# Performance work log

Hardware: AMD Instinct MI355X
Metric: run time of the kernel (lower is better)

The kernel has to match this reference:

```python
import jax, jax.numpy as jnp
import numpy as np

# Geometry constants fixed by the source's index arithmetic
GRID_P, GRID_Q, NUM_ANCH = 60, 40, 9   # p = (i//9)%60, q = i//(60*9), sr = i%9
N = GRID_P * GRID_Q * NUM_ANCH          # 21600 anchors per image
K = 1000                                # top-K candidates kept before NMS
MAX_BOXES = 18                          # fixed output boxes per image
THRESH = 0.5                            # NMS overlap threshold
BATCH = 64


def setup_inputs() -> dict:
    key = jax.random.key(0)
    k1, k2 = jax.random.split(key)
    x = jax.random.normal(k1, (BATCH, N, 6), dtype=jnp.float32)
    # anchor boxes (x, y, w, h); keep w,h strictly positive and away from 0
    anchor_boxes = jax.random.uniform(k2, (GRID_P, GRID_Q, NUM_ANCH, 4),
                                      dtype=jnp.float32, minval=0.05, maxval=1.0)
    return {"x": x, "anchor_boxes": anchor_boxes}


def _per_sample(ypred, anchors):
    scores, order = jax.lax.top_k(ypred[:, 0], K)          # descending, matches tf.argsort DESC [:1000]
    p = (order // NUM_ANCH) % GRID_P
    q = order // (GRID_P * NUM_ANCH)
    sr = order % NUM_ANCH
    a = anchors[p, q, sr]                                   # [K, 4] (xa, ya, wa, ha)
    regr = ypred[order, 2:6]                                # [K, 4] (dx, dy, dw, dh)
    xc = regr[:, 0] * a[:, 2] + a[:, 0]
    yc = regr[:, 1] * a[:, 3] + a[:, 1]
    w = a[:, 2] * jnp.exp(regr[:, 2])
    h = a[:, 3] * jnp.exp(regr[:, 3])
    cand = jnp.stack([xc, yc, w, h, scores], axis=-1)       # [K, 5] xywh+score

    # xywh -> xyxy for overlap computation (as in non_max_suppression_fast)
    x1 = xc - 0.5 * w; x2 = xc + 0.5 * w
    y1 = yc - 0.5 * h; y2 = yc + 0.5 * h
    area = (x2 - x1) * (y2 - y1)                            # [K]

    # pairwise intersection; overlap[i, j] = inter(i, j) / area(j)  (source divides by
    # the area of the lower-scored candidate, NOT the union -- kept faithfully)
    xx1 = jnp.maximum(x1[:, None], x1[None, :])
    yy1 = jnp.maximum(y1[:, None], y1[None, :])
    xx2 = jnp.minimum(x2[:, None], x2[None, :])
    yy2 = jnp.minimum(y2[:, None], y2[None, :])
    iw = jnp.maximum(0.0, xx2 - xx1)
    ih = jnp.maximum(0.0, yy2 - yy1)
    sup = (iw * ih / area[None, :]) > THRESH                # [K, K] bool

    # greedy NMS over candidates in descending-score order
    jrange = jnp.arange(K)
    def body(i, keep):
        return keep & ~(keep[i] & sup[i] & (jrange > i))
    keep = jax.lax.fori_loop(0, K, body, jnp.ones((K,), dtype=bool))

    # pack first MAX_BOXES kept boxes into fixed-shape output
    ranks = jnp.cumsum(keep) - 1                            # position among kept
    valid = keep & (ranks < MAX_BOXES)
    picked = jnp.zeros((MAX_BOXES, 5), cand.dtype).at[
        jnp.where(valid, ranks, MAX_BOXES)
    ].set(jnp.where(valid[:, None], cand, 0.0), mode='drop')

    # pad with top-scored decoded boxes if fewer than MAX_BOXES survive NMS
    n = jnp.minimum(jnp.sum(keep), MAX_BOXES)
    j = jnp.arange(MAX_BOXES)
    pad = cand[jnp.clip(j - n, 0, K - 1)]
    return jnp.where((j < n)[:, None], picked, pad)         # [MAX_BOXES, 5]


def reference(x, anchor_boxes):
    return jax.vmap(lambda y: _per_sample(y, anchor_boxes))(x)  # [B, 18, 5]
```

## Files before the change

### kernel.cpp

```cpp
#include <hip/hip_runtime.h>

#define NELEM 21600
#define KSEL 1000
#define MAXB 18
#define NT 1024
#define CAP 2048
#define NCHUNK 4
#define QC 8100
#define NFULL 21
#define NTAIL (NELEM - NFULL * NT)

typedef unsigned long long ull;

__device__ __forceinline__ unsigned fkey(float f) {
  unsigned u = __float_as_uint(f);
  return (u & 0x80000000u) ? ~u : (u | 0x80000000u);
}
__device__ __forceinline__ float unfkey(unsigned k) {
  unsigned u = (k & 0x80000000u) ? (k ^ 0x80000000u) : ~k;
  return __uint_as_float(u);
}

__global__ __launch_bounds__(NT) void k1_scan(
    const float* __restrict__ x, unsigned* __restrict__ gkeys,
    unsigned* __restrict__ ghist) {
  const int blk = blockIdx.x;
  const int s = blk / NCHUNK, c = blk % NCHUNK;
  const int t = threadIdx.x;
  const float4* xq = (const float4*)(x + (size_t)s * NELEM * 6);
  unsigned* gk = gkeys + (size_t)s * NELEM;

  __shared__ unsigned h[2048];
  h[2 * t] = 0u; h[2 * t + 1] = 0u;
  __syncthreads();

  const int base = c * QC;
  #pragma unroll
  for (int k = 0; k < 7; ++k) {
    int g = base + t + (k << 10);
    float4 v = xq[g];
    int r = g % 3;
    if (r == 0) {
      unsigned key = fkey(v.x);
      gk[2 * (g / 3)] = key;
      atomicAdd(&h[key >> 21], 1u);
    } else if (r == 1) {
      unsigned key = fkey(v.z);
      gk[2 * (g / 3) + 1] = key;
      atomicAdd(&h[key >> 21], 1u);
    }
  }
  if (t < QC - 7 * 1024) {
    int g = base + t + (7 << 10);
    float4 v = xq[g];
    int r = g % 3;
    if (r == 0) {
      unsigned key = fkey(v.x);
      gk[2 * (g / 3)] = key;
      atomicAdd(&h[key >> 21], 1u);
    } else if (r == 1) {
      unsigned key = fkey(v.z);
      gk[2 * (g / 3) + 1] = key;
      atomicAdd(&h[key >> 21], 1u);
    }
  }
  __syncthreads();
  unsigned* gh = ghist + (size_t)blk * 2048;
  gh[2 * t] = h[2 * t];
  gh[2 * t + 1] = h[2 * t + 1];
}

__device__ void select_bucket(const unsigned* hist, unsigned target,
                              volatile unsigned* chunkSuf,
                              unsigned* outB, unsigned* outCnt, unsigned* outAbove) {
  const int tid = threadIdx.x;
  const int w = tid >> 6, l = tid & 63;
  unsigned h1 = hist[w * 128 + 2 * l + 1];
  unsigned s = hist[w * 128 + 2 * l] + h1;
  #pragma unroll
  for (int d = 1; d < 64; d <<= 1) {
    unsigned t = __shfl_down(s, d);
    if (l + d < 64) s += t;
  }
  if (l == 0) chunkSuf[w] = s;
  __syncthreads();
  if (w == 0) {
    unsigned ct = (l < 16) ? chunkSuf[l] : 0u;
    unsigned cs = ct;
    #pragma unroll
    for (int d = 1; d < 16; d <<= 1) {
      unsigned t = __shfl_down(cs, d);
      if (l + d < 16) cs += t;
    }
    if (l < 16) chunkSuf[l] = cs - ct;
  }
  __syncthreads();
  unsigned base = chunkSuf[w];
  unsigned sufE = s + base;
  unsigned sN = __shfl_down(s, 1);
  unsigned sufN = ((l < 63) ? sN : 0u) + base;
  unsigned geOdd = sufN + h1;
  if (sufE >= target && geOdd < target) { *outB = w * 128u + 2u * l;     *outCnt = sufE;  *outAbove = geOdd; }
  if (geOdd >= target && sufN < target) { *outB = w * 128u + 2u * l + 1; *outCnt = geOdd; *outAbove = sufN;  }
  __syncthreads();
}

__global__ __launch_bounds__(NT, 4) void k2a_sort(
    const unsigned* __restrict__ gkeys, const unsigned* __restrict__ ghist,
    ull* __restrict__ gsort) {
  const int s = blockIdx.x;
  const int tid = threadIdx.x;
  const unsigned* ks = gkeys + (size_t)s * NELEM;

  __shared__ unsigned hist[2048];
  __shared__ unsigned chunkSuf[16];
  __shared__ ull selPk[CAP];
  __shared__ unsigned sB, sCnt, sAbove;
  __shared__ unsigned baseKey;
  __shared__ unsigned cnt;

  unsigned kv[NFULL];
  #pragma unroll
  for (int u = 0; u < NFULL; ++u) kv[u] = ks[tid + (u << 10)];
  unsigned ktail = 0u;
  const bool hastail = tid < NTAIL;
  if (hastail) ktail = ks[tid + NFULL * NT];
  asm volatile("" :
      "+v"(kv[0]), "+v"(kv[1]), "+v"(kv[2]), "+v"(kv[3]), "+v"(kv[4]),
      "+v"(kv[5]), "+v"(kv[6]), "+v"(kv[7]), "+v"(kv[8]), "+v"(kv[9]),
      "+v"(kv[10]), "+v"(kv[11]), "+v"(kv[12]), "+v"(kv[13]), "+v"(kv[14]),
      "+v"(kv[15]), "+v"(kv[16]), "+v"(kv[17]), "+v"(kv[18]), "+v"(kv[19]),
      "+v"(kv[20]), "+v"(ktail));

  {
    unsigned h0 = 0, h1 = 0;
    #pragma unroll
    for (int c = 0; c < NCHUNK; ++c) {
      const unsigned* gh = ghist + (size_t)(s * NCHUNK + c) * 2048;
      h0 += gh[2 * tid];
      h1 += gh[2 * tid + 1];
    }
    hist[2 * tid] = h0; hist[2 * tid + 1] = h1;
  }
  __syncthreads();
  select_bucket(hist, KSEL, chunkSuf, &sB, &sCnt, &sAbove);
  const unsigned b1 = sB, cnt1 = sCnt, above1 = sAbove;

  if (cnt1 > 1024) {
    hist[2 * tid] = 0u; hist[2 * tid + 1] = 0u;
    __syncthreads();
    #pragma unroll
    for (int u = 0; u < NFULL; ++u)
      if ((kv[u] >> 21) == b1) atomicAdd(&hist[(kv[u] >> 10) & 0x7FFu], 1u);
    if (hastail && (ktail >> 21) == b1) atomicAdd(&hist[(ktail >> 10) & 0x7FFu], 1u);
    __syncthreads();
    select_bucket(hist, KSEL - above1, chunkSuf, &sB, &sCnt, &sAbove);
    if (tid == 0) { baseKey = (b1 << 21) | (sB << 10); cnt = 0u; }
  } else {
    if (tid == 0) { baseKey = b1 << 21; cnt = 0u; }
  }
  __syncthreads();

  const unsigned TB = baseKey;
  const int lw = tid & 63;
  #pragma unroll
  for (int u = 0; u < NFULL; ++u) {
    bool pred = kv[u] >= TB;
    ull mask = __ballot(pred);
    if (mask) {
      int leader = __builtin_ctzll(mask);
      unsigned total = (unsigned)__popcll(mask);
      unsigned basep = 0;
      if (lw == leader) basep = atomicAdd(&cnt, total);
      basep = __shfl(basep, leader);
      if (pred) {
        unsigned p = basep + (unsigned)__popcll(mask & ((1ull << lw) - 1ull));
        unsigned i = (unsigned)(tid + (u << 10));
        if (p < CAP) selPk[p] = ((ull)kv[u] << 32) | (unsigned)(~i);
      }
    }
  }
  if (hastail && ktail >= TB) {
    unsigned p = atomicAdd(&cnt, 1u);
    unsigned i = (unsigned)(tid + NFULL * NT);
    if (p < CAP) selPk[p] = ((ull)ktail << 32) | (unsigned)(~i);
  }
  __syncthreads();
  const unsigned realCnt = (cnt < CAP) ? cnt : CAP;
  const unsigned P = (realCnt <= 1024u) ? 1024u : 2048u;
  for (unsigned i = realCnt + tid; i < P; i += NT) selPk[i] = 0ull;
  __syncthreads();

  if (P == 1024u) {
    ull a = selPk[tid];
    #pragma unroll
    for (unsigned k = 2; k <= 64; k <<= 1) {
      #pragma unroll
      for (unsigned j = k >> 1; j >= 1; j >>= 1) {
        bool up = ((tid & k) == 0);
        bool lower = ((tid & j) == 0);
        bool takeMax = (up == lower);
        ull o = __shfl_xor(a, (int)j);
        a = takeMax ? (a > o ? a : o) : (a < o ? a : o);
      }
    }
    selPk[tid] = a;
    __syncthreads();
    for (unsigned k = 128; k <= 1024; k <<= 1) {
      for (unsigned j = k >> 1; j >= 64; j >>= 1) {
        if (tid < 512) {
          unsigned p = (unsigned)tid;
          unsigned vi = ((p & ~(j - 1)) << 1) | (p & (j - 1));
          unsigned li = vi | j;
          ull av = selPk[vi], cv = selPk[li];
          bool doswap = ((vi & k) == 0) ? (av < cv) : (av > cv);
          if (doswap) { selPk[vi] = cv; selPk[li] = av; }
        }
        __syncthreads();
      }
      a = selPk[tid];
      {
        bool up = ((tid & k) == 0);
        #pragma unroll
        for (unsigned j = 32; j >= 1; j >>= 1) {
          bool lower = ((tid & j) == 0);
          bool takeMax = (up == lower);
          ull o = __shfl_xor(a, (int)j);
          a = takeMax ? (a > o ? a : o) : (a < o ? a : o);
        }
      }
      selPk[tid] = a;
      __syncthreads();
    }
  } else {
    const int w = tid >> 6, L = tid & 63;
    const int ea = (w << 7) | (L << 1);
    ull a = selPk[ea], bb = selPk[ea + 1];
    #pragma unroll
    for (unsigned k = 2; k <= 128; k <<= 1) {
      #pragma unroll
      for (unsigned j = k >> 1; j >= 2; j >>= 1) {
        bool up = ((ea & k) == 0);
        bool lower = ((ea & j) == 0);
        bool takeMax = (up == lower);
        ull oa = __shfl_xor(a, (int)(j >> 1));
        ull ob = __shfl_xor(bb, (int)(j >> 1));
        a  = takeMax ? (a  > oa ? a  : oa) : (a  < oa ? a  : oa);
        bb = takeMax ? (bb > ob ? bb : ob) : (bb < ob ? bb : ob);
      }
      bool up = ((ea & k) == 0);
      ull mx = a > bb ? a : bb, mn = a > bb ? bb : a;
      a = up ? mx : mn; bb = up ? mn : mx;
    }
    selPk[ea] = a; selPk[ea + 1] = bb;
    __syncthreads();
    for (unsigned k = 256; k <= 2048; k <<= 1) {
      for (unsigned j = k >> 1; j >= 128; j >>= 1) {
        unsigned p = (unsigned)tid;
        unsigned vi = ((p & ~(j - 1)) << 1) | (p & (j - 1));
        unsigned li = vi | j;
        ull av = selPk[vi], cv = selPk[li];
        bool doswap = ((vi & k) == 0) ? (av < cv) : (av > cv);
        if (doswap) { selPk[vi] = cv; selPk[li] = av; }
        __syncthreads();
      }
      a = selPk[ea]; bb = selPk[ea + 1];
      bool up = (((unsigned)(w << 7) & k) == 0);
      #pragma unroll
      for (unsigned j = 64; j >= 2; j >>= 1) {
        bool lower = ((ea & j) == 0);
        bool takeMax = (up == lower);
        ull oa = __shfl_xor(a, (int)(j >> 1));
        ull ob = __shfl_xor(bb, (int)(j >> 1));
        a  = takeMax ? (a  > oa ? a  : oa) : (a  < oa ? a  : oa);
        bb = takeMax ? (bb > ob ? bb : ob) : (bb < ob ? bb : ob);
      }
      ull mx = a > bb ? a : bb, mn = a > bb ? bb : a;
      a = up ? mx : mn; bb = up ? mn : mx;
      selPk[ea] = a; selPk[ea + 1] = bb;
      __syncthreads();
    }
  }

  gsort[(size_t)s * 1024 + tid] = selPk[tid];
}

__global__ __launch_bounds__(NT, 2) void k2b_nms(
    const float* __restrict__ x, const float* __restrict__ anch,
    const ull* __restrict__ gsort, float* __restrict__ out) {
  const int s = blockIdx.x;
  const int tid = threadIdx.x;
  const float* xb = x + (size_t)s * NELEM * 6;

  __shared__ ull pkL[1024];
  __shared__ float px1[64 * 17], py1[64 * 17], px2[64 * 17], py2[64 * 17], par[64 * 17];
  __shared__ int keptRank[MAXB];
  __shared__ int numKept;

  ull pk = gsort[(size_t)s * 1024 + tid];
  pkL[tid] = pk;
  if (tid < KSEL) {
    unsigned idx = ~(unsigned)pk;
    const float2* e2 = (const float2*)(xb + (size_t)idx * 6 + 2);
    float2 ra = e2[0], rb = e2[1];
    unsigned pp = (idx / 9u) % 60u;
    unsigned qq = idx / 540u;
    unsigned sr = idx % 9u;
    const float* ap = anch + (((pp * 40u + qq) * 9u + sr) * 4u);
    float ax = ap[0], ay = ap[1], aw = ap[2], ah = ap[3];
    float xc = ra.x * aw + ax;
    float yc = ra.y * ah + ay;
    float w = aw * expf(rb.x);
    float h = ah * expf(rb.y);
    float x1 = xc - 0.5f * w, x2 = xc + 0.5f * w;
    float y1 = yc - 0.5f * h, y2 = yc + 0.5f * h;
    int a = (tid >> 4) * 17 + (tid & 15);
    px1[a] = x1; py1[a] = y1; px2[a] = x2; py2[a] = y2;
    par[a] = (x2 - x1) * (y2 - y1);
  }
  __syncthreads();

  if (tid < 64) {
    const int lane = tid;
    float X1[16], Y1[16], X2[16], Y2[16], AR[16];
    unsigned alive = 0u;
    #pragma unroll
    for (int ss = 0; ss < 16; ++ss) {
      int r = lane * 16 + ss;
      int a = lane * 17 + ss;
      X1[ss] = px1[a]; Y1[ss] = py1[a];
      X2[ss] = px2[a]; Y2[ss] = py2[a]; AR[ss] = par[a];
      alive |= (r < KSEL ? 1u : 0u) << ss;
    }
    int nk = 0;
    while (nk < MAXB) {
      ull bal = __ballot(alive != 0u);
      if (!bal) break;
      int F = __builtin_ctzll(bal);
      int myss = (int)__builtin_ctz(alive | 0x10000u);
      int ssw = __shfl(myss, F);
      int m = F * 16 + ssw;
      if (lane == 0) keptRank[nk] = m;
      int am = (m >> 4) * 17 + (m & 15);
      float wx1 = px1[am], wy1 = py1[am], wx2 = px2[am], wy2 = py2[am];
      ++nk;
      if (nk >= MAXB) break;
      #pragma unroll
      for (int ss = 0; ss < 16; ++ss) {
        if (alive & (1u << ss)) {
          float iw = fmaxf(fminf(X2[ss], wx2) - fmaxf(X1[ss], wx1), 0.f);
          float ih = fmaxf(fminf(Y2[ss], wy2) - fmaxf(Y1[ss], wy1), 0.f);
          if (iw * ih / AR[ss] > 0.5f) alive &= ~(1u << ss);
        }
      }
    }
    if (lane == 0) numKept = nk;
  }
  __syncthreads();

  const int n = numKept;
  if (tid < MAXB) {
    int j = tid;
    int r = (j < n) ? keptRank[j] : (j - n);
    ull pkr = pkL[r];
    unsigned idx = ~(unsigned)pkr;
    float sc = unfkey((unsigned)(pkr >> 32));
    const float2* e2 = (const float2*)(xb + (size_t)idx * 6 + 2);
    float2 ra = e2[0], rb = e2[1];
    unsigned pp = (idx / 9u) % 60u;
    unsigned qq = idx / 540u;
    unsigned sr = idx % 9u;
    const float* ap = anch + (((pp * 40u + qq) * 9u + sr) * 4u);
    float ax = ap[0], ay = ap[1], aw = ap[2], ah = ap[3];
    float xc = ra.x * aw + ax;
    float yc = ra.y * ah + ay;
    float w = aw * expf(rb.x);
    float h = ah * expf(rb.y);
    float* o = out + s * (MAXB * 5) + j * 5;
    o[0] = xc; o[1] = yc; o[2] = w; o[3] = h; o[4] = sc;
  }
}

extern "C" void kernel_launch(void* const* d_in, const int* in_sizes, int n_in,
                              void* d_out, int out_size, void* d_ws, size_t ws_size,
                              hipStream_t stream) {
  const float* x = (const float*)d_in[0];
  const float* anch = (const float*)d_in[1];
  float* out = (float*)d_out;
  const int B = in_sizes[0] / (NELEM * 6);
  unsigned* ghist = (unsigned*)d_ws;
  unsigned* gkeys = ghist + (size_t)B * NCHUNK * 2048;
  ull* gsort = (ull*)(gkeys + (size_t)B * NELEM);
  k1_scan<<<dim3(B * NCHUNK), dim3(NT), 0, stream>>>(x, gkeys, ghist);
  k2a_sort<<<dim3(B), dim3(NT), 0, stream>>>(gkeys, ghist, gsort);
  k2b_nms<<<dim3(B), dim3(NT), 0, stream>>>(x, anch, gsort, out);
}
```

Measured before the change: 58.68 us.

## Fuse sort and NMS kernels with a small top-96 fast path and fallback

```diff
diff --git a/kernel.cpp b/kernel.cpp
--- a/kernel.cpp
+++ b/kernel.cpp
@@ -5,6 +5,8 @@
 #define MAXB 18
 #define NT 1024
 #define CAP 2048
+#define TARGF 96
+#define CAPF 256
 #define NCHUNK 4
 #define QC 8100
 #define NFULL 21
@@ -105,19 +107,24 @@
   __syncthreads();
 }
 
-__global__ __launch_bounds__(NT, 4) void k2a_sort(
+__global__ __launch_bounds__(NT) void k2_fused(
+    const float* __restrict__ x, const float* __restrict__ anch,
     const unsigned* __restrict__ gkeys, const unsigned* __restrict__ ghist,
-    ull* __restrict__ gsort) {
+    float* __restrict__ out) {
   const int s = blockIdx.x;
   const int tid = threadIdx.x;
+  const float* xb = x + (size_t)s * NELEM * 6;
   const unsigned* ks = gkeys + (size_t)s * NELEM;
 
   __shared__ unsigned hist[2048];
   __shared__ unsigned chunkSuf[16];
   __shared__ ull selPk[CAP];
+  __shared__ float px1[1088], py1[1088], px2[1088], py2[1088], par[1088];
   __shared__ unsigned sB, sCnt, sAbove;
-  __shared__ unsigned baseKey;
-  __shared__ unsigned cnt;
+  __shared__ unsigned baseKey, cnt;
+  __shared__ int keptRank[MAXB];
+  __shared__ int numKept;
+  __shared__ int fb;
 
   unsigned kv[NFULL];
   #pragma unroll
@@ -125,6 +132,22 @@
   unsigned ktail = 0u;
   const bool hastail = tid < NTAIL;
   if (hastail) ktail = ks[tid + NFULL * NT];
+
+  {
+    unsigned h0 = 0, h1 = 0;
+    #pragma unroll
+    for (int c = 0; c < NCHUNK; ++c) {
+      const unsigned* gh = ghist + (size_t)(s * NCHUNK + c) * 2048;
+      h0 += gh[2 * tid];
+      h1 += gh[2 * tid + 1];
+    }
+    hist[2 * tid] = h0; hist[2 * tid + 1] = h1;
+  }
+  if (tid == 0) fb = 0;
+  __syncthreads();
+  select_bucket(hist, TARGF, chunkSuf, &sB, &sCnt, &sAbove);
+  const unsigned b1 = sB, cnt1 = sCnt, above1 = sAbove;
+
   asm volatile("" :
       "+v"(kv[0]), "+v"(kv[1]), "+v"(kv[2]), "+v"(kv[3]), "+v"(kv[4]),
       "+v"(kv[5]), "+v"(kv[6]), "+v"(kv[7]), "+v"(kv[8]), "+v"(kv[9]),
@@ -132,21 +155,9 @@
       "+v"(kv[15]), "+v"(kv[16]), "+v"(kv[17]), "+v"(kv[18]), "+v"(kv[19]),
       "+v"(kv[20]), "+v"(ktail));
 
-  {
-    unsigned h0 = 0, h1 = 0;
-    #pragma unroll
-    for (int c = 0; c < NCHUNK; ++c) {
-      const unsigned* gh = ghist + (size_t)(s * NCHUNK + c) * 2048;
-      h0 += gh[2 * tid];
-      h1 += gh[2 * tid + 1];
-    }
-    hist[2 * tid] = h0; hist[2 * tid + 1] = h1;
-  }
-  __syncthreads();
-  select_bucket(hist, KSEL, chunkSuf, &sB, &sCnt, &sAbove);
-  const unsigned b1 = sB, cnt1 = sCnt, above1 = sAbove;
-
-  if (cnt1 > 1024) {
+  if (cnt1 <= CAPF) {
+    if (tid == 0) { baseKey = b1 << 21; cnt = 0u; }
+  } else {
     hist[2 * tid] = 0u; hist[2 * tid + 1] = 0u;
     __syncthreads();
     #pragma unroll
@@ -154,61 +165,65 @@
       if ((kv[u] >> 21) == b1) atomicAdd(&hist[(kv[u] >> 10) & 0x7FFu], 1u);
     if (hastail && (ktail >> 21) == b1) atomicAdd(&hist[(ktail >> 10) & 0x7FFu], 1u);
     __syncthreads();
-    select_bucket(hist, KSEL - above1, chunkSuf, &sB, &sCnt, &sAbove);
+    select_bucket(hist, TARGF - above1, chunkSuf, &sB, &sCnt, &sAbove);
     if (tid == 0) { baseKey = (b1 << 21) | (sB << 10); cnt = 0u; }
-  } else {
-    if (tid == 0) { baseKey = b1 << 21; cnt = 0u; }
-  }
-  __syncthreads();
-
-  const unsigned TB = baseKey;
-  const int lw = tid & 63;
-  #pragma unroll
-  for (int u = 0; u < NFULL; ++u) {
-    bool pred = kv[u] >= TB;
-    ull mask = __ballot(pred);
-    if (mask) {
-      int leader = __builtin_ctzll(mask);
-      unsigned total = (unsigned)__popcll(mask);
-      unsigned basep = 0;
-      if (lw == leader) basep = atomicAdd(&cnt, total);
-      basep = __shfl(basep, leader);
-      if (pred) {
-        unsigned p = basep + (unsigned)__popcll(mask & ((1ull << lw) - 1ull));
-        unsigned i = (unsigned)(tid + (u << 10));
-        if (p < CAP) selPk[p] = ((ull)kv[u] << 32) | (unsigned)(~i);
-      }
-    }
-  }
-  if (hastail && ktail >= TB) {
-    unsigned p = atomicAdd(&cnt, 1u);
-    unsigned i = (unsigned)(tid + NFULL * NT);
-    if (p < CAP) selPk[p] = ((ull)ktail << 32) | (unsigned)(~i);
-  }
-  __syncthreads();
-  const unsigned realCnt = (cnt < CAP) ? cnt : CAP;
-  const unsigned P = (realCnt <= 1024u) ? 1024u : 2048u;
-  for (unsigned i = realCnt + tid; i < P; i += NT) selPk[i] = 0ull;
-  __syncthreads();
-
-  if (P == 1024u) {
-    ull a = selPk[tid];
-    #pragma unroll
-    for (unsigned k = 2; k <= 64; k <<= 1) {
+  }
+  __syncthreads();
+
+  {
+    const unsigned TB = baseKey;
+    const int lw = tid & 63;
+    #pragma unroll
+    for (int u = 0; u < NFULL; ++u) {
+      bool pred = kv[u] >= TB;
+      ull mask = __ballot(pred);
+      if (mask) {
+        int leader = __builtin_ctzll(mask);
+        unsigned total = (unsigned)__popcll(mask);
+        unsigned basep = 0;
+        if (lw == leader) basep = atomicAdd(&cnt, total);
+        basep = __shfl(basep, leader);
+        if (pred) {
+          unsigned p = basep + (unsigned)__popcll(mask & ((1ull << lw) - 1ull));
+          unsigned i = (unsigned)(tid + (u << 10));
+          if (p < CAPF) selPk[p] = ((ull)kv[u] << 32) | (unsigned)(~i);
+        }
+      }
+    }
+    if (hastail && ktail >= TB) {
+      unsigned p = atomicAdd(&cnt, 1u);
+      unsigned i = (unsigned)(tid + NFULL * NT);
+      if (p < CAPF) selPk[p] = ((ull)ktail << 32) | (unsigned)(~i);
+    }
+  }
+  __syncthreads();
+  const unsigned cntS = cnt;
+  if (tid == 0 && cntS > CAPF) fb = 1;
+  __syncthreads();
+
+  if (!fb) {
+    for (unsigned i = cntS + tid; i < CAPF; i += NT) selPk[i] = 0ull;
+    __syncthreads();
+
+    if (tid < 256) {
+      ull a = selPk[tid];
       #pragma unroll
-      for (unsigned j = k >> 1; j >= 1; j >>= 1) {
-        bool up = ((tid & k) == 0);
-        bool lower = ((tid & j) == 0);
-        bool takeMax = (up == lower);
-        ull o = __shfl_xor(a, (int)j);
-        a = takeMax ? (a > o ? a : o) : (a < o ? a : o);
-      }
-    }
-    selPk[tid] = a;
-    __syncthreads();
-    for (unsigned k = 128; k <= 1024; k <<= 1) {
+      for (unsigned k = 2; k <= 64; k <<= 1) {
+        #pragma unroll
+        for (unsigned j = k >> 1; j >= 1; j >>= 1) {
+          bool up = ((tid & k) == 0);
+          bool lower = ((tid & j) == 0);
+          bool takeMax = (up == lower);
+          ull o = __shfl_xor(a, (int)j);
+          a = takeMax ? (a > o ? a : o) : (a < o ? a : o);
+        }
+      }
+      selPk[tid] = a;
+    }
+    __syncthreads();
+    for (unsigned k = 128; k <= 256; k <<= 1) {
       for (unsigned j = k >> 1; j >= 64; j >>= 1) {
-        if (tid < 512) {
+        if (tid < 128) {
           unsigned p = (unsigned)tid;
           unsigned vi = ((p & ~(j - 1)) << 1) | (p & (j - 1));
           unsigned li = vi | j;
@@ -218,8 +233,8 @@
         }
         __syncthreads();
       }
-      a = selPk[tid];
-      {
+      if (tid < 256) {
+        ull a = selPk[tid];
         bool up = ((tid & k) == 0);
         #pragma unroll
         for (unsigned j = 32; j >= 1; j >>= 1) {
@@ -228,11 +243,157 @@
           ull o = __shfl_xor(a, (int)j);
           a = takeMax ? (a > o ? a : o) : (a < o ? a : o);
         }
-      }
-      selPk[tid] = a;
+        selPk[tid] = a;
+      }
       __syncthreads();
     }
+
+    if (tid < (int)cntS) {
+      unsigned idx = ~(unsigned)selPk[tid];
+      const float2* e2 = (const float2*)(xb + (size_t)idx * 6 + 2);
+      float2 ra = e2[0], rb = e2[1];
+      unsigned pp = (idx / 9u) % 60u;
+      unsigned qq = idx / 540u;
+      unsigned sr = idx % 9u;
+      const float* ap = anch + (((pp * 40u + qq) * 9u + sr) * 4u);
+      float ax = ap[0], ay = ap[1], aw = ap[2], ah = ap[3];
+      float xc = ra.x * aw + ax;
+      float yc = ra.y * ah + ay;
+      float w = aw * expf(rb.x);
+      float h = ah * expf(rb.y);
+      float x1 = xc - 0.5f * w, x2 = xc + 0.5f * w;
+      float y1 = yc - 0.5f * h, y2 = yc + 0.5f * h;
+      int a = (tid >> 4) * 17 + (tid & 15);
+      px1[a] = x1; py1[a] = y1; px2[a] = x2; py2[a] = y2;
+      par[a] = (x2 - x1) * (y2 - y1);
+    }
+    __syncthreads();
+
+    if (tid < 64) {
+      const int lane = tid;
+      float X1[4], Y1[4], X2[4], Y2[4], AR[4];
+      unsigned alive = 0u;
+      #pragma unroll
+      for (int ss = 0; ss < 4; ++ss) {
+        int r = lane * 4 + ss;
+        int a = (r >> 4) * 17 + (r & 15);
+        X1[ss] = px1[a]; Y1[ss] = py1[a];
+        X2[ss] = px2[a]; Y2[ss] = py2[a]; AR[ss] = par[a];
+        alive |= (r < (int)cntS ? 1u : 0u) << ss;
+      }
+      int nk = 0;
+      while (nk < MAXB) {
+        ull bal = __ballot(alive != 0u);
+        if (!bal) break;
+        int F = __builtin_ctzll(bal);
+        int myss = (int)__builtin_ctz(alive | 0x10u);
+        int ssw = __shfl(myss, F);
+        int m = F * 4 + ssw;
+        if (lane == 0) keptRank[nk] = m;
+        int am = (m >> 4) * 17 + (m & 15);
+        float wx1 = px1[am], wy1 = py1[am], wx2 = px2[am], wy2 = py2[am];
+        ++nk;
+        if (nk >= MAXB) break;
+        #pragma unroll
+        for (int ss = 0; ss < 4; ++ss) {
+          if (alive & (1u << ss)) {
+            float iw = fmaxf(fminf(X2[ss], wx2) - fmaxf(X1[ss], wx1), 0.f);
+            float ih = fmaxf(fminf(Y2[ss], wy2) - fmaxf(Y1[ss], wy1), 0.f);
+            if (iw * ih / AR[ss] > 0.5f) alive &= ~(1u << ss);
+          }
+        }
+      }
+      if (lane == 0) {
+        numKept = nk;
+        if (nk < MAXB) fb = 1;
+      }
+    }
+    __syncthreads();
+  }
+
+  if (!fb) {
+    if (tid < MAXB) {
+      int j = tid;
+      int n = numKept;
+      int r = (j < n) ? keptRank[j] : (j - n);
+      ull pk = selPk[r];
+      unsigned idx = ~(unsigned)pk;
+      float sc = unfkey((unsigned)(pk >> 32));
+      const float2* e2 = (const float2*)(xb + (size_t)idx * 6 + 2);
+      float2 ra = e2[0], rb = e2[1];
+      unsigned pp = (idx / 9u) % 60u;
+      unsigned qq = idx / 540u;
+      unsigned sr = idx % 9u;
+      const float* ap = anch + (((pp * 40u + qq) * 9u + sr) * 4u);
+      float ax = ap[0], ay = ap[1], aw = ap[2], ah = ap[3];
+      float xc = ra.x * aw + ax;
+      float yc = ra.y * ah + ay;
+      float w = aw * expf(rb.x);
+      float h = ah * expf(rb.y);
+      float* o = out + s * (MAXB * 5) + j * 5;
+      o[0] = xc; o[1] = yc; o[2] = w; o[3] = h; o[4] = sc;
+    }
+    return;
+  }
+
+  hist[2 * tid] = 0u; hist[2 * tid + 1] = 0u;
+  __syncthreads();
+  #pragma unroll
+  for (int u = 0; u < NFULL; ++u) atomicAdd(&hist[kv[u] >> 21], 1u);
+  if (hastail) atomicAdd(&hist[ktail >> 21], 1u);
+  __syncthreads();
+  select_bucket(hist, KSEL, chunkSuf, &sB, &sCnt, &sAbove);
+  const unsigned fb1 = sB, fcnt1 = sCnt, fabove1 = sAbove;
+
+  if (fcnt1 > CAP) {
+    hist[2 * tid] = 0u; hist[2 * tid + 1] = 0u;
+    __syncthreads();
+    #pragma unroll
+    for (int u = 0; u < NFULL; ++u)
+      if ((kv[u] >> 21) == fb1) atomicAdd(&hist[(kv[u] >> 10) & 0x7FFu], 1u);
+    if (hastail && (ktail >> 21) == fb1) atomicAdd(&hist[(ktail >> 10) & 0x7FFu], 1u);
+    __syncthreads();
+    select_bucket(hist, KSEL - fabove1, chunkSuf, &sB, &sCnt, &sAbove);
+    if (tid == 0) { baseKey = (fb1 << 21) | (sB << 10); cnt = 0u; }
   } else {
+    if (tid == 0) { baseKey = fb1 << 21; cnt = 0u; }
+  }
+  __syncthreads();
+
+  {
+    const unsigned TB = baseKey;
+    const int lw = tid & 63;
+    #pragma unroll
+    for (int u = 0; u < NFULL; ++u) {
+      bool pred = kv[u] >= TB;
+      ull mask = __ballot(pred);
+      if (mask) {
+        int leader = __builtin_ctzll(mask);
+        unsigned total = (unsigned)__popcll(mask);
+        unsigned basep = 0;
+        if (lw == leader) basep = atomicAdd(&cnt, total);
+        basep = __shfl(basep, leader);
+        if (pred) {
+          unsigned p = basep + (unsigned)__popcll(mask & ((1ull << lw) - 1ull));
+          unsigned i = (unsigned)(tid + (u << 10));
+          if (p < CAP) selPk[p] = ((ull)kv[u] << 32) | (unsigned)(~i);
+        }
+      }
+    }
+    if (hastail && ktail >= TB) {
+      unsigned p = atomicAdd(&cnt, 1u);
+      unsigned i = (unsigned)(tid + NFULL * NT);
+      if (p < CAP) selPk[p] = ((ull)ktail << 32) | (unsigned)(~i);
+    }
+  }
+  __syncthreads();
+  {
+    const unsigned realCnt = (cnt < CAP) ? cnt : CAP;
+    for (unsigned i = realCnt + tid; i < CAP; i += NT) selPk[i] = 0ull;
+  }
+  __syncthreads();
+
+  {
     const int w = tid >> 6, L = tid & 63;
     const int ea = (w << 7) | (L << 1);
     ull a = selPk[ea], bb = selPk[ea + 1];
@@ -282,25 +443,8 @@
     }
   }
 
-  gsort[(size_t)s * 1024 + tid] = selPk[tid];
-}
-
-__global__ __launch_bounds__(NT, 2) void k2b_nms(
-    const float* __restrict__ x, const float* __restrict__ anch,
-    const ull* __restrict__ gsort, float* __restrict__ out) {
-  const int s = blockIdx.x;
-  const int tid = threadIdx.x;
-  const float* xb = x + (size_t)s * NELEM * 6;
-
-  __shared__ ull pkL[1024];
-  __shared__ float px1[64 * 17], py1[64 * 17], px2[64 * 17], py2[64 * 17], par[64 * 17];
-  __shared__ int keptRank[MAXB];
-  __shared__ int numKept;
-
-  ull pk = gsort[(size_t)s * 1024 + tid];
-  pkL[tid] = pk;
   if (tid < KSEL) {
-    unsigned idx = ~(unsigned)pk;
+    unsigned idx = ~(unsigned)selPk[tid];
     const float2* e2 = (const float2*)(xb + (size_t)idx * 6 + 2);
     float2 ra = e2[0], rb = e2[1];
     unsigned pp = (idx / 9u) % 60u;
@@ -358,13 +502,13 @@
   }
   __syncthreads();
 
-  const int n = numKept;
   if (tid < MAXB) {
     int j = tid;
+    int n = numKept;
     int r = (j < n) ? keptRank[j] : (j - n);
-    ull pkr = pkL[r];
-    unsigned idx = ~(unsigned)pkr;
-    float sc = unfkey((unsigned)(pkr >> 32));
+    ull pk = selPk[r];
+    unsigned idx = ~(unsigned)pk;
+    float sc = unfkey((unsigned)(pk >> 32));
     const float2* e2 = (const float2*)(xb + (size_t)idx * 6 + 2);
     float2 ra = e2[0], rb = e2[1];
     unsigned pp = (idx / 9u) % 60u;
@@ -390,8 +534,6 @@
   const int B = in_sizes[0] / (NELEM * 6);
   unsigned* ghist = (unsigned*)d_ws;
   unsigned* gkeys = ghist + (size_t)B * NCHUNK * 2048;
-  ull* gsort = (ull*)(gkeys + (size_t)B * NELEM);
   k1_scan<<<dim3(B * NCHUNK), dim3(NT), 0, stream>>>(x, gkeys, ghist);
-  k2a_sort<<<dim3(B), dim3(NT), 0, stream>>>(gkeys, ghist, gsort);
-  k2b_nms<<<dim3(B), dim3(NT), 0, stream>>>(x, anch, gsort, out);
+  k2_fused<<<dim3(B), dim3(NT), 0, stream>>>(x, anch, gkeys, ghist, out);
 }
```

After: 73.80 us. 25.8% more time.

## Fuse sort and NMS kernels, single-wave register bitonic sort, split scan finer

Applied to the files above, without the earlier changes.

```diff
diff --git a/kernel.cpp b/kernel.cpp
--- a/kernel.cpp
+++ b/kernel.cpp
@@ -5,8 +5,8 @@
 #define MAXB 18
 #define NT 1024
 #define CAP 2048
-#define NCHUNK 4
-#define QC 8100
+#define NCHUNK 8
+#define QC 4050
 #define NFULL 21
 #define NTAIL (NELEM - NFULL * NT)
 
@@ -20,6 +20,10 @@
   unsigned u = (k & 0x80000000u) ? (k ^ 0x80000000u) : ~k;
   return __uint_as_float(u);
 }
+
+#define K1PROC(v, g) { int r = (g) % 3; \
+  if (r == 0) { unsigned key = fkey((v).x); gk[2 * ((g) / 3)] = key; atomicAdd(&h[key >> 21], 1u); } \
+  else if (r == 1) { unsigned key = fkey((v).z); gk[2 * ((g) / 3) + 1] = key; atomicAdd(&h[key >> 21], 1u); } }
 
 __global__ __launch_bounds__(NT) void k1_scan(
     const float* __restrict__ x, unsigned* __restrict__ gkeys,
@@ -32,38 +36,24 @@
 
   __shared__ unsigned h[2048];
   h[2 * t] = 0u; h[2 * t + 1] = 0u;
-  __syncthreads();
 
   const int base = c * QC;
-  #pragma unroll
-  for (int k = 0; k < 7; ++k) {
-    int g = base + t + (k << 10);
-    float4 v = xq[g];
-    int r = g % 3;
-    if (r == 0) {
-      unsigned key = fkey(v.x);
-      gk[2 * (g / 3)] = key;
-      atomicAdd(&h[key >> 21], 1u);
-    } else if (r == 1) {
-      unsigned key = fkey(v.z);
-      gk[2 * (g / 3) + 1] = key;
-      atomicAdd(&h[key >> 21], 1u);
-    }
-  }
-  if (t < QC - 7 * 1024) {
-    int g = base + t + (7 << 10);
-    float4 v = xq[g];
-    int r = g % 3;
-    if (r == 0) {
-      unsigned key = fkey(v.x);
-      gk[2 * (g / 3)] = key;
-      atomicAdd(&h[key >> 21], 1u);
-    } else if (r == 1) {
-      unsigned key = fkey(v.z);
-      gk[2 * (g / 3) + 1] = key;
-      atomicAdd(&h[key >> 21], 1u);
-    }
-  }
+  float4 va0 = xq[base + t];
+  float4 va1 = xq[base + t + 1024];
+  float4 va2 = xq[base + t + 2048];
+  const bool hast = t < (QC - 3072);
+  float4 vt = hast ? xq[base + t + 3072] : va0;
+  asm volatile("" :
+      "+v"(va0.x), "+v"(va0.y), "+v"(va0.z), "+v"(va0.w),
+      "+v"(va1.x), "+v"(va1.y), "+v"(va1.z), "+v"(va1.w),
+      "+v"(va2.x), "+v"(va2.y), "+v"(va2.z), "+v"(va2.w),
+      "+v"(vt.x), "+v"(vt.y), "+v"(vt.z), "+v"(vt.w));
+  __syncthreads();
+
+  { int g = base + t;        K1PROC(va0, g) }
+  { int g = base + t + 1024; K1PROC(va1, g) }
+  { int g = base + t + 2048; K1PROC(va2, g) }
+  if (hast) { int g = base + t + 3072; K1PROC(vt, g) }
   __syncthreads();
   unsigned* gh = ghist + (size_t)blk * 2048;
   gh[2 * t] = h[2 * t];
@@ -105,19 +95,23 @@
   __syncthreads();
 }
 
-__global__ __launch_bounds__(NT, 4) void k2a_sort(
+__global__ __launch_bounds__(NT, 4) void k2_main(
+    const float* __restrict__ x, const float* __restrict__ anch,
     const unsigned* __restrict__ gkeys, const unsigned* __restrict__ ghist,
-    ull* __restrict__ gsort) {
+    float* __restrict__ out) {
   const int s = blockIdx.x;
   const int tid = threadIdx.x;
+  const float* xb = x + (size_t)s * NELEM * 6;
   const unsigned* ks = gkeys + (size_t)s * NELEM;
 
   __shared__ unsigned hist[2048];
   __shared__ unsigned chunkSuf[16];
   __shared__ ull selPk[CAP];
+  __shared__ float px1[1088], py1[1088], px2[1088], py2[1088], par[1088];
   __shared__ unsigned sB, sCnt, sAbove;
-  __shared__ unsigned baseKey;
-  __shared__ unsigned cnt;
+  __shared__ unsigned baseKey, cnt;
+  __shared__ int keptRank[MAXB];
+  __shared__ int numKept;
 
   unsigned kv[NFULL];
   #pragma unroll
@@ -125,26 +119,27 @@
   unsigned ktail = 0u;
   const bool hastail = tid < NTAIL;
   if (hastail) ktail = ks[tid + NFULL * NT];
+
+  {
+    unsigned h0 = 0, h1 = 0;
+    #pragma unroll
+    for (int c = 0; c < NCHUNK; ++c) {
+      const unsigned* gh = ghist + (size_t)(s * NCHUNK + c) * 2048;
+      h0 += gh[2 * tid];
+      h1 += gh[2 * tid + 1];
+    }
+    hist[2 * tid] = h0; hist[2 * tid + 1] = h1;
+  }
+  __syncthreads();
+  select_bucket(hist, KSEL, chunkSuf, &sB, &sCnt, &sAbove);
+  const unsigned b1 = sB, cnt1 = sCnt, above1 = sAbove;
+
   asm volatile("" :
       "+v"(kv[0]), "+v"(kv[1]), "+v"(kv[2]), "+v"(kv[3]), "+v"(kv[4]),
       "+v"(kv[5]), "+v"(kv[6]), "+v"(kv[7]), "+v"(kv[8]), "+v"(kv[9]),
       "+v"(kv[10]), "+v"(kv[11]), "+v"(kv[12]), "+v"(kv[13]), "+v"(kv[14]),
       "+v"(kv[15]), "+v"(kv[16]), "+v"(kv[17]), "+v"(kv[18]), "+v"(kv[19]),
       "+v"(kv[20]), "+v"(ktail));
-
-  {
-    unsigned h0 = 0, h1 = 0;
-    #pragma unroll
-    for (int c = 0; c < NCHUNK; ++c) {
-      const unsigned* gh = ghist + (size_t)(s * NCHUNK + c) * 2048;
-      h0 += gh[2 * tid];
-      h1 += gh[2 * tid + 1];
-    }
-    hist[2 * tid] = h0; hist[2 * tid + 1] = h1;
-  }
-  __syncthreads();
-  select_bucket(hist, KSEL, chunkSuf, &sB, &sCnt, &sAbove);
-  const unsigned b1 = sB, cnt1 = sCnt, above1 = sAbove;
 
   if (cnt1 > 1024) {
     hist[2 * tid] = 0u; hist[2 * tid + 1] = 0u;
@@ -161,77 +156,77 @@
   }
   __syncthreads();
 
-  const unsigned TB = baseKey;
-  const int lw = tid & 63;
-  #pragma unroll
-  for (int u = 0; u < NFULL; ++u) {
-    bool pred = kv[u] >= TB;
-    ull mask = __ballot(pred);
-    if (mask) {
-      int leader = __builtin_ctzll(mask);
-      unsigned total = (unsigned)__popcll(mask);
-      unsigned basep = 0;
-      if (lw == leader) basep = atomicAdd(&cnt, total);
-      basep = __shfl(basep, leader);
-      if (pred) {
-        unsigned p = basep + (unsigned)__popcll(mask & ((1ull << lw) - 1ull));
-        unsigned i = (unsigned)(tid + (u << 10));
-        if (p < CAP) selPk[p] = ((ull)kv[u] << 32) | (unsigned)(~i);
-      }
-    }
-  }
-  if (hastail && ktail >= TB) {
-    unsigned p = atomicAdd(&cnt, 1u);
-    unsigned i = (unsigned)(tid + NFULL * NT);
-    if (p < CAP) selPk[p] = ((ull)ktail << 32) | (unsigned)(~i);
-  }
-  __syncthreads();
-  const unsigned realCnt = (cnt < CAP) ? cnt : CAP;
-  const unsigned P = (realCnt <= 1024u) ? 1024u : 2048u;
-  for (unsigned i = realCnt + tid; i < P; i += NT) selPk[i] = 0ull;
-  __syncthreads();
-
-  if (P == 1024u) {
-    ull a = selPk[tid];
-    #pragma unroll
-    for (unsigned k = 2; k <= 64; k <<= 1) {
-      #pragma unroll
-      for (unsigned j = k >> 1; j >= 1; j >>= 1) {
-        bool up = ((tid & k) == 0);
-        bool lower = ((tid & j) == 0);
-        bool takeMax = (up == lower);
-        ull o = __shfl_xor(a, (int)j);
-        a = takeMax ? (a > o ? a : o) : (a < o ? a : o);
-      }
-    }
-    selPk[tid] = a;
+  {
+    const unsigned TB = baseKey;
+    const int lw = tid & 63;
+    #pragma unroll
+    for (int u = 0; u < NFULL; ++u) {
+      bool pred = kv[u] >= TB;
+      ull mask = __ballot(pred);
+      if (mask) {
+        int leader = __builtin_ctzll(mask);
+        unsigned total = (unsigned)__popcll(mask);
+        unsigned basep = 0;
+        if (lw == leader) basep = atomicAdd(&cnt, total);
+        basep = __shfl(basep, leader);
+        if (pred) {
+          unsigned p = basep + (unsigned)__popcll(mask & ((1ull << lw) - 1ull));
+          unsigned i = (unsigned)(tid + (u << 10));
+          if (p < CAP) selPk[p] = ((ull)kv[u] << 32) | (unsigned)(~i);
+        }
+      }
+    }
+    if (hastail && ktail >= TB) {
+      unsigned p = atomicAdd(&cnt, 1u);
+      unsigned i = (unsigned)(tid + NFULL * NT);
+      if (p < CAP) selPk[p] = ((ull)ktail << 32) | (unsigned)(~i);
+    }
+  }
+  __syncthreads();
+  const unsigned cntS = (cnt < CAP) ? cnt : CAP;
+  for (unsigned i = cntS + tid; i < CAP; i += NT) selPk[i] = 0ull;
+  __syncthreads();
+
+  if (cntS <= 1024u) {
+    if (tid < 64) {
+      const int lane = tid;
+      ull v[16];
+      #pragma unroll
+      for (int r = 0; r < 16; ++r) v[r] = selPk[(r << 6) | lane];
+      #pragma unroll
+      for (unsigned k = 2; k <= 1024; k <<= 1) {
+        #pragma unroll
+        for (unsigned j = k >> 1; j >= 1; j >>= 1) {
+          if (j >= 64) {
+            const int rb = (int)(j >> 6);
+            #pragma unroll
+            for (int r = 0; r < 16; ++r) {
+              if ((r & rb) == 0) {
+                const int r2 = r | rb;
+                bool up = ((((unsigned)r << 6) & k) == 0);
+                ull a = v[r], b = v[r2];
+                ull mx = a > b ? a : b, mn = a > b ? b : a;
+                v[r]  = up ? mx : mn;
+                v[r2] = up ? mn : mx;
+              }
+            }
+          } else {
+            #pragma unroll
+            for (int r = 0; r < 16; ++r) {
+              unsigned e = ((unsigned)r << 6) | (unsigned)lane;
+              bool up = ((e & k) == 0);
+              bool lower = (((unsigned)lane & j) == 0);
+              bool takeMax = (up == lower);
+              ull o = __shfl_xor(v[r], (int)j);
+              v[r] = takeMax ? (v[r] > o ? v[r] : o) : (v[r] < o ? v[r] : o);
+            }
+          }
+        }
+      }
+      #pragma unroll
+      for (int r = 0; r < 16; ++r) selPk[(r << 6) | lane] = v[r];
+    }
     __syncthreads();
-    for (unsigned k = 128; k <= 1024; k <<= 1) {
-      for (unsigned j = k >> 1; j >= 64; j >>= 1) {
-        if (tid < 512) {
-          unsigned p = (unsigned)tid;
-          unsigned vi = ((p & ~(j - 1)) << 1) | (p & (j - 1));
-          unsigned li = vi | j;
-          ull av = selPk[vi], cv = selPk[li];
-          bool doswap = ((vi & k) == 0) ? (av < cv) : (av > cv);
-          if (doswap) { selPk[vi] = cv; selPk[li] = av; }
-        }
-        __syncthreads();
-      }
-      a = selPk[tid];
-      {
-        bool up = ((tid & k) == 0);
-        #pragma unroll
-        for (unsigned j = 32; j >= 1; j >>= 1) {
-          bool lower = ((tid & j) == 0);
-          bool takeMax = (up == lower);
-          ull o = __shfl_xor(a, (int)j);
-          a = takeMax ? (a > o ? a : o) : (a < o ? a : o);
-        }
-      }
-      selPk[tid] = a;
-      __syncthreads();
-    }
   } else {
     const int w = tid >> 6, L = tid & 63;
     const int ea = (w << 7) | (L << 1);
@@ -282,25 +277,8 @@
     }
   }
 
-  gsort[(size_t)s * 1024 + tid] = selPk[tid];
-}
-
-__global__ __launch_bounds__(NT, 2) void k2b_nms(
-    const float* __restrict__ x, const float* __restrict__ anch,
-    const ull* __restrict__ gsort, float* __restrict__ out) {
-  const int s = blockIdx.x;
-  const int tid = threadIdx.x;
-  const float* xb = x + (size_t)s * NELEM * 6;
-
-  __shared__ ull pkL[1024];
-  __shared__ float px1[64 * 17], py1[64 * 17], px2[64 * 17], py2[64 * 17], par[64 * 17];
-  __shared__ int keptRank[MAXB];
-  __shared__ int numKept;
-
-  ull pk = gsort[(size_t)s * 1024 + tid];
-  pkL[tid] = pk;
   if (tid < KSEL) {
-    unsigned idx = ~(unsigned)pk;
+    unsigned idx = ~(unsigned)selPk[tid];
     const float2* e2 = (const float2*)(xb + (size_t)idx * 6 + 2);
     float2 ra = e2[0], rb = e2[1];
     unsigned pp = (idx / 9u) % 60u;
@@ -362,9 +340,9 @@
   if (tid < MAXB) {
     int j = tid;
     int r = (j < n) ? keptRank[j] : (j - n);
-    ull pkr = pkL[r];
-    unsigned idx = ~(unsigned)pkr;
-    float sc = unfkey((unsigned)(pkr >> 32));
+    ull pk = selPk[r];
+    unsigned idx = ~(unsigned)pk;
+    float sc = unfkey((unsigned)(pk >> 32));
     const float2* e2 = (const float2*)(xb + (size_t)idx * 6 + 2);
     float2 ra = e2[0], rb = e2[1];
     unsigned pp = (idx / 9u) % 60u;
@@ -390,8 +368,6 @@
   const int B = in_sizes[0] / (NELEM * 6);
   unsigned* ghist = (unsigned*)d_ws;
   unsigned* gkeys = ghist + (size_t)B * NCHUNK * 2048;
-  ull* gsort = (ull*)(gkeys + (size_t)B * NELEM);
   k1_scan<<<dim3(B * NCHUNK), dim3(NT), 0, stream>>>(x, gkeys, ghist);
-  k2a_sort<<<dim3(B), dim3(NT), 0, stream>>>(gkeys, ghist, gsort);
-  k2b_nms<<<dim3(B), dim3(NT), 0, stream>>>(x, anch, gsort, out);
-}
+  k2_main<<<dim3(B), dim3(NT), 0, stream>>>(x, anch, gkeys, ghist, out);
+}
```

New measurement: 86.15 us. +46.8%, slower.
